# Performance work log

Hardware: AMD Instinct MI355X
Metric: run time of the kernel (lower is better)

The kernel has to match this reference:

```python
import jax, jax.numpy as jnp
import numpy as np

H = 64  # hidden_size
IN = 1  # input_size
OUT = 32  # fc output


def _lstm_layer(x, Wih, Whh, bih, bhh):
    """x: (B,T,D_in). Returns (outputs (B,T,H), final h (B,H)). PyTorch gate order i,f,g,o."""
    B = x.shape[0]
    b = bih + bhh  # (4H,)
    # precompute input contributions for all timesteps: (T,B,4H)
    xW = jnp.einsum('btd,gd->tbg', x, Wih) + b

    def step(carry, xw_t):
        h, c = carry
        gates = xw_t + h @ Whh.T  # (B,4H)
        i, f, g, o = jnp.split(gates, 4, axis=-1)
        i = jax.nn.sigmoid(i)
        f = jax.nn.sigmoid(f)
        g = jnp.tanh(g)
        o = jax.nn.sigmoid(o)
        c = f * c + i * g
        h = o * jnp.tanh(c)
        return (h, c), h

    h0 = jnp.zeros((B, H), dtype=x.dtype)
    c0 = jnp.zeros((B, H), dtype=x.dtype)
    (h_T, _), hs = jax.lax.scan(step, (h0, c0), xW)
    return jnp.swapaxes(hs, 0, 1), h_T


def setup_inputs() -> dict:
    key = jax.random.key(0)
    ks = jax.random.split(key, 11)
    s_ih0 = 1.0 / np.sqrt(H)
    inp = {
        'x': jax.random.normal(ks[0], (2048, 512, IN), dtype=jnp.float32),
        # layer 0: input_size -> H
        'Wih0': jax.random.uniform(ks[1], (4 * H, IN), minval=-s_ih0, maxval=s_ih0),
        'Whh0': jax.random.uniform(ks[2], (4 * H, H), minval=-s_ih0, maxval=s_ih0),
        'bih0': jax.random.uniform(ks[3], (4 * H,), minval=-s_ih0, maxval=s_ih0),
        'bhh0': jax.random.uniform(ks[4], (4 * H,), minval=-s_ih0, maxval=s_ih0),
        # layer 1: H -> H
        'Wih1': jax.random.uniform(ks[5], (4 * H, H), minval=-s_ih0, maxval=s_ih0),
        'Whh1': jax.random.uniform(ks[6], (4 * H, H), minval=-s_ih0, maxval=s_ih0),
        'bih1': jax.random.uniform(ks[7], (4 * H,), minval=-s_ih0, maxval=s_ih0),
        'bhh1': jax.random.uniform(ks[8], (4 * H,), minval=-s_ih0, maxval=s_ih0),
        # fc: H -> 32
        'fcW': jax.random.uniform(ks[9], (OUT, H), minval=-s_ih0, maxval=s_ih0),
        'fcb': jax.random.uniform(ks[10], (OUT,), minval=-s_ih0, maxval=s_ih0),
    }
    return inp


def reference(x, Wih0, Whh0, bih0, bhh0, Wih1, Whh1, bih1, bhh1, fcW, fcb):
    h1_seq, _ = _lstm_layer(x, Wih0, Whh0, bih0, bhh0)
    _, h_last = _lstm_layer(h1_seq, Wih1, Whh1, bih1, bhh1)  # hidden[-1]
    features = jax.nn.relu(h_last @ fcW.T + fcb)  # (B, 32)
    return features
```

## Files before the change

kernel.cpp:

```cpp
#include <hip/hip_runtime.h>
#include <hip/hip_bf16.h>


#define HID 64
#define TSTEPS 512
#define MB 8
#define RS 80

typedef _Float16 f16x8 __attribute__((ext_vector_type(8)));
typedef float f32x4 __attribute__((ext_vector_type(4)));
typedef float f32x2 __attribute__((ext_vector_type(2)));

#define KSIG (-1.44269504089f)
#define KTANH (2.88539008178f)

__global__ __launch_bounds__(512, 2) void lstm_feat_kernel(
    const float* __restrict__ x,
    const float* __restrict__ Wih0, const float* __restrict__ Whh0,
    const float* __restrict__ bih0, const float* __restrict__ bhh0,
    const float* __restrict__ Wih1, const float* __restrict__ Whh1,
    const float* __restrict__ bih1, const float* __restrict__ bhh1,
    const float* __restrict__ fcW, const float* __restrict__ fcb,
    float* __restrict__ out)
{
    __shared__ float x_lds[TSTEPS * MB];
    __shared__ __align__(16) _Float16 h0_lds[2][MB * RS];
    __shared__ __align__(16) _Float16 h1_lds[2][MB * RS];
    __shared__ float h1f32[MB * HID];
    __shared__ float fcw_lds[32 * HID];
    __shared__ float fcb_lds[32];

    const int tid  = threadIdx.x;
    const int wave = tid >> 6;
    const int lane = tid & 63;
    const int nq   = lane & 15;
    const int quad = lane >> 4;
    const bool l0q = quad < 2;
    const bool evn = (nq & 1) == 0;
    const int ucell = wave * 8 + (nq >> 1);
    const int bbase = blockIdx.x * MB;

    for (int i = tid; i < TSTEPS * MB; i += 512) {
        int r = i >> 9, t = i & (TSTEPS - 1);
        x_lds[t * MB + r] = x[(bbase + r) * TSTEPS + t];
    }
    for (int i = tid; i < 32 * HID; i += 512) fcw_lds[i] = fcW[i];
    if (tid < 32) fcb_lds[tid] = fcb[tid];
    for (int i = tid; i < 2 * MB * RS; i += 512) {
        ((_Float16*)h0_lds)[i] = (_Float16)0.f;
        ((_Float16*)h1_lds)[i] = (_Float16)0.f;
    }

    const int nA = (nq & 1) * 64 + ucell;
    const int nB = (2 + (nq & 1)) * 64 + ucell;
    const float kBs = evn ? KTANH : KSIG;
    f16x8 wA0[2], wB0[2], wiA[2], whA[2], wiB[2], whB[2];
    #pragma unroll
    for (int ks = 0; ks < 2; ++ks) {
        const int k0 = quad * 8 + ks * 32;
        f16x8 a, b, c, d, e, f;
        #pragma unroll
        for (int j = 0; j < 8; ++j) {
            a[j] = (_Float16)(KSIG * Whh0[nA * HID + k0 + j]);
            b[j] = (_Float16)(kBs  * Whh0[nB * HID + k0 + j]);
            c[j] = (_Float16)(KSIG * Wih1[nA * HID + k0 + j]);
            d[j] = (_Float16)(KSIG * Whh1[nA * HID + k0 + j]);
            e[j] = (_Float16)(kBs  * Wih1[nB * HID + k0 + j]);
            f[j] = (_Float16)(kBs  * Whh1[nB * HID + k0 + j]);
        }
        wA0[ks] = a; wB0[ks] = b; wiA[ks] = c; whA[ks] = d; wiB[ks] = e; whB[ks] = f;
    }
    const float bA0 = KSIG * (bih0[nA] + bhh0[nA]);
    const float bB0 = kBs  * (bih0[nB] + bhh0[nB]);
    const float bA1 = KSIG * (bih1[nA] + bhh1[nA]);
    const float bB1 = kBs  * (bih1[nB] + bhh1[nB]);
    const float wxA = KSIG * Wih0[nA];
    const float wxB = kBs  * Wih0[nB];

    const float AB = evn ? -2.f : 1.f;
    const float BB = evn ? 1.f : 0.f;

    const f32x4 biasA1 = {bA1, bA1, bA1, bA1};
    const f32x4 biasB1 = {bB1, bB1, bB1, bB1};
    const int arow = (nq & 7) * RS + quad * 8;
    const int xoff = (quad & 1) * 4;

    const int e0 = evn ? 0 : 2;
    const int b0 = (quad * 4 + e0) & 7;
    const int waddr = b0 * RS + ucell;
    _Float16* const hdw[2] = { l0q ? h0_lds[1] : h1_lds[1],
                               l0q ? h0_lds[0] : h1_lds[0] };

    f32x2 cst2 = {0.f, 0.f};
    float hl0 = 0.f, hl1 = 0.f;

    __syncthreads();

    f32x4 cA, cB;
    {
        const float4 xv = *(const float4*)&x_lds[0 * MB + xoff];
        cA[0] = fmaf(xv.x, wxA, bA0); cA[1] = fmaf(xv.y, wxA, bA0);
        cA[2] = fmaf(xv.z, wxA, bA0); cA[3] = fmaf(xv.w, wxA, bA0);
        cB[0] = fmaf(xv.x, wxB, bB0); cB[1] = fmaf(xv.y, wxB, bB0);
        cB[2] = fmaf(xv.z, wxB, bB0); cB[3] = fmaf(xv.w, wxB, bB0);
    }

    auto step = [&](int xk_next, int pp, bool maskK0) {
        const f16x8 a00 = *(const f16x8*)&h0_lds[pp][arow];
        const f16x8 a01 = *(const f16x8*)&h0_lds[pp][arow + 32];
        const f16x8 a10 = *(const f16x8*)&h1_lds[pp][arow];
        const f16x8 a11 = *(const f16x8*)&h1_lds[pp][arow + 32];

        f32x4 tA = __builtin_amdgcn_mfma_f32_16x16x32_f16(a00, wA0[0], cA, 0, 0, 0);
        f32x4 tB = __builtin_amdgcn_mfma_f32_16x16x32_f16(a00, wB0[0], cB, 0, 0, 0);
        f32x4 uA = __builtin_amdgcn_mfma_f32_16x16x32_f16(a00, wiA[0], biasA1, 0, 0, 0);
        f32x4 uB = __builtin_amdgcn_mfma_f32_16x16x32_f16(a00, wiB[0], biasB1, 0, 0, 0);
        tA = __builtin_amdgcn_mfma_f32_16x16x32_f16(a01, wA0[1], tA, 0, 0, 0);
        tB = __builtin_amdgcn_mfma_f32_16x16x32_f16(a01, wB0[1], tB, 0, 0, 0);
        uA = __builtin_amdgcn_mfma_f32_16x16x32_f16(a01, wiA[1], uA, 0, 0, 0);
        uB = __builtin_amdgcn_mfma_f32_16x16x32_f16(a01, wiB[1], uB, 0, 0, 0);
        uA = __builtin_amdgcn_mfma_f32_16x16x32_f16(a10, whA[0], uA, 0, 0, 0);
        uB = __builtin_amdgcn_mfma_f32_16x16x32_f16(a10, whB[0], uB, 0, 0, 0);
        uA = __builtin_amdgcn_mfma_f32_16x16x32_f16(a11, whA[1], uA, 0, 0, 0);
        uB = __builtin_amdgcn_mfma_f32_16x16x32_f16(a11, whB[1], uB, 0, 0, 0);

        {
            const float4 xv = *(const float4*)&x_lds[xk_next * MB + xoff];
            cA[0] = fmaf(xv.x, wxA, bA0); cA[1] = fmaf(xv.y, wxA, bA0);
            cA[2] = fmaf(xv.z, wxA, bA0); cA[3] = fmaf(xv.w, wxA, bA0);
            cB[0] = fmaf(xv.x, wxB, bB0); cB[1] = fmaf(xv.y, wxB, bB0);
            cB[2] = fmaf(xv.z, wxB, bB0); cB[3] = fmaf(xv.w, wxB, bB0);
        }

        const bool docell = maskK0 ? l0q : true;
        if (docell) {
            float sA[4], sB[4];
            #pragma unroll
            for (int r = 0; r < 4; ++r) {
                const float pA = l0q ? tA[r] : uA[r];
                const float pB = l0q ? tB[r] : uB[r];
                sA[r] = __builtin_amdgcn_rcpf(1.f + __builtin_amdgcn_exp2f(pA));
                sB[r] = fmaf(AB, __builtin_amdgcn_rcpf(1.f + __builtin_amdgcn_exp2f(pB)), BB);
            }
            const float rxA0 = __shfl_xor(evn ? sA[2] : sA[0], 1);
            const float rxA1 = __shfl_xor(evn ? sA[3] : sA[1], 1);
            const float rxB0 = __shfl_xor(evn ? sB[2] : sB[0], 1);
            const float rxB1 = __shfl_xor(evn ? sB[3] : sB[1], 1);
            f32x2 iv2, fv2, gv2, ov2;
            iv2.x = evn ? sA[0] : rxA0;  iv2.y = evn ? sA[1] : rxA1;
            fv2.x = evn ? rxA0 : sA[2];  fv2.y = evn ? rxA1 : sA[3];
            gv2.x = evn ? sB[0] : rxB0;  gv2.y = evn ? sB[1] : rxB1;
            ov2.x = evn ? rxB0 : sB[2];  ov2.y = evn ? rxB1 : sB[3];
            cst2 = fv2 * cst2 + iv2 * gv2;
            f32x2 ex, rc;
            ex.x = __builtin_amdgcn_exp2f(KTANH * cst2.x);
            ex.y = __builtin_amdgcn_exp2f(KTANH * cst2.y);
            rc.x = __builtin_amdgcn_rcpf(1.f + ex.x);
            rc.y = __builtin_amdgcn_rcpf(1.f + ex.y);
            const f32x2 th = 1.f - 2.f * rc;
            const f32x2 h2 = ov2 * th;
            hl0 = h2.x; hl1 = h2.y;
            _Float16* hdst = (pp == 0) ? hdw[0] : hdw[1];
            hdst[waddr]      = (_Float16)h2.x;
            hdst[waddr + RS] = (_Float16)h2.y;
        }
        __syncthreads();
    };

    step(1, 0, true);
    for (int k = 1; k < 511; k += 2) {
        step(k + 1, 1, false);
        step(k + 2, 0, false);
    }
    step(511, 1, false);
    step(511, 0, false);

    if (!l0q) {
        h1f32[b0 * HID + ucell]       = hl0;
        h1f32[(b0 + 1) * HID + ucell] = hl1;
    }
    __syncthreads();

    if (tid < MB * 32) {
        const int o  = tid & 31;
        const int rr = tid >> 5;
        float acc = fcb_lds[o];
        #pragma unroll 8
        for (int kk = 0; kk < HID; ++kk)
            acc += h1f32[rr * HID + kk] * fcw_lds[o * HID + kk];
        out[(bbase + rr) * 32 + o] = fmaxf(acc, 0.f);
    }
}

extern "C" void kernel_launch(void* const* d_in, const int* in_sizes, int n_in,
                              void* d_out, int out_size, void* d_ws, size_t ws_size,
                              hipStream_t stream) {
    const float* x    = (const float*)d_in[0];
    const float* Wih0 = (const float*)d_in[1];
    const float* Whh0 = (const float*)d_in[2];
    const float* bih0 = (const float*)d_in[3];
    const float* bhh0 = (const float*)d_in[4];
    const float* Wih1 = (const float*)d_in[5];
    const float* Whh1 = (const float*)d_in[6];
    const float* bih1 = (const float*)d_in[7];
    const float* bhh1 = (const float*)d_in[8];
    const float* fcW  = (const float*)d_in[9];
    const float* fcb  = (const float*)d_in[10];
    float* out = (float*)d_out;

    lstm_feat_kernel<<<2048 / MB, 512, 0, stream>>>(
        x, Wih0, Whh0, bih0, bhh0, Wih1, Whh1, bih1, bhh1, fcW, fcb, out);
}
```

Before: 378.1 us.

## Split gate columns across 16 waves, one gate per lane per MFMA tile

Doubles the block to 1024 threads so each wave handles 4 hidden units with all four gates in one 16-column MFMA tile. Each wave now issues 6 MFMAs per step instead of 12, and each lane updates a single cell state. Gate values are gathered with two xor-shuffle rounds instead of one. The aim is to shorten the per-step serial critical path of the recurrence by spreading work over more waves. The cost is more waves joining each per-step barrier, an extra shuffle round, and lower occupancy per CU.

```diff
diff --git a/kernel.cpp b/kernel.cpp
--- a/kernel.cpp
+++ b/kernel.cpp
@@ -9,12 +9,11 @@
 
 typedef _Float16 f16x8 __attribute__((ext_vector_type(8)));
 typedef float f32x4 __attribute__((ext_vector_type(4)));
-typedef float f32x2 __attribute__((ext_vector_type(2)));
 
 #define KSIG (-1.44269504089f)
 #define KTANH (2.88539008178f)
 
-__global__ __launch_bounds__(512, 2) void lstm_feat_kernel(
+__global__ __launch_bounds__(1024, 4) void lstm_feat_kernel(
     const float* __restrict__ x,
     const float* __restrict__ Wih0, const float* __restrict__ Whh0,
     const float* __restrict__ bih0, const float* __restrict__ bhh0,
@@ -36,73 +35,58 @@
     const int nq   = lane & 15;
     const int quad = lane >> 4;
     const bool l0q = quad < 2;
-    const bool evn = (nq & 1) == 0;
-    const int ucell = wave * 8 + (nq >> 1);
+    const int gate = nq & 3;
+    const int u    = wave * 4 + (nq >> 2);
     const int bbase = blockIdx.x * MB;
 
-    for (int i = tid; i < TSTEPS * MB; i += 512) {
+    for (int i = tid; i < TSTEPS * MB; i += 1024) {
         int r = i >> 9, t = i & (TSTEPS - 1);
         x_lds[t * MB + r] = x[(bbase + r) * TSTEPS + t];
     }
-    for (int i = tid; i < 32 * HID; i += 512) fcw_lds[i] = fcW[i];
+    for (int i = tid; i < 32 * HID; i += 1024) fcw_lds[i] = fcW[i];
     if (tid < 32) fcb_lds[tid] = fcb[tid];
-    for (int i = tid; i < 2 * MB * RS; i += 512) {
+    for (int i = tid; i < 2 * MB * RS; i += 1024) {
         ((_Float16*)h0_lds)[i] = (_Float16)0.f;
         ((_Float16*)h1_lds)[i] = (_Float16)0.f;
     }
 
-    const int nA = (nq & 1) * 64 + ucell;
-    const int nB = (2 + (nq & 1)) * 64 + ucell;
-    const float kBs = evn ? KTANH : KSIG;
-    f16x8 wA0[2], wB0[2], wiA[2], whA[2], wiB[2], whB[2];
+    const int nW = gate * 64 + u;
+    const float kg = (gate == 2) ? KTANH : KSIG;
+    f16x8 wh0[2], wi1[2], wh1[2];
     #pragma unroll
     for (int ks = 0; ks < 2; ++ks) {
         const int k0 = quad * 8 + ks * 32;
-        f16x8 a, b, c, d, e, f;
+        f16x8 a, b, c;
         #pragma unroll
         for (int j = 0; j < 8; ++j) {
-            a[j] = (_Float16)(KSIG * Whh0[nA * HID + k0 + j]);
-            b[j] = (_Float16)(kBs  * Whh0[nB * HID + k0 + j]);
-            c[j] = (_Float16)(KSIG * Wih1[nA * HID + k0 + j]);
-            d[j] = (_Float16)(KSIG * Whh1[nA * HID + k0 + j]);
-            e[j] = (_Float16)(kBs  * Wih1[nB * HID + k0 + j]);
-            f[j] = (_Float16)(kBs  * Whh1[nB * HID + k0 + j]);
+            a[j] = (_Float16)(kg * Whh0[nW * HID + k0 + j]);
+            b[j] = (_Float16)(kg * Wih1[nW * HID + k0 + j]);
+            c[j] = (_Float16)(kg * Whh1[nW * HID + k0 + j]);
         }
-        wA0[ks] = a; wB0[ks] = b; wiA[ks] = c; whA[ks] = d; wiB[ks] = e; whB[ks] = f;
+        wh0[ks] = a; wi1[ks] = b; wh1[ks] = c;
     }
-    const float bA0 = KSIG * (bih0[nA] + bhh0[nA]);
-    const float bB0 = kBs  * (bih0[nB] + bhh0[nB]);
-    const float bA1 = KSIG * (bih1[nA] + bhh1[nA]);
-    const float bB1 = kBs  * (bih1[nB] + bhh1[nB]);
-    const float wxA = KSIG * Wih0[nA];
-    const float wxB = kBs  * Wih0[nB];
+    const float b0c = kg * (bih0[nW] + bhh0[nW]);
+    const float b1c = kg * (bih1[nW] + bhh1[nW]);
+    const float wxc = kg * Wih0[nW];
+    const float Ag = (gate == 2) ? -2.f : 1.f;
+    const float Bg = (gate == 2) ? 1.f : 0.f;
 
-    const float AB = evn ? -2.f : 1.f;
-    const float BB = evn ? 1.f : 0.f;
-
-    const f32x4 biasA1 = {bA1, bA1, bA1, bA1};
-    const f32x4 biasB1 = {bB1, bB1, bB1, bB1};
+    const f32x4 bias1 = {b1c, b1c, b1c, b1c};
     const int arow = (nq & 7) * RS + quad * 8;
     const int xoff = (quad & 1) * 4;
-
-    const int e0 = evn ? 0 : 2;
-    const int b0 = (quad * 4 + e0) & 7;
-    const int waddr = b0 * RS + ucell;
-    _Float16* const hdw[2] = { l0q ? h0_lds[1] : h1_lds[1],
-                               l0q ? h0_lds[0] : h1_lds[0] };
-
-    f32x2 cst2 = {0.f, 0.f};
-    float hl0 = 0.f, hl1 = 0.f;
+    const int bcell = (quad * 4 + gate) & 7;
+    const int waddr = bcell * RS + u;
+    const bool tlo = (gate & 1) != 0;
+    const bool thi = (gate & 2) != 0;
+    float cst = 0.f, hl = 0.f;
 
     __syncthreads();
 
-    f32x4 cA, cB;
+    f32x4 cA;
     {
         const float4 xv = *(const float4*)&x_lds[0 * MB + xoff];
-        cA[0] = fmaf(xv.x, wxA, bA0); cA[1] = fmaf(xv.y, wxA, bA0);
-        cA[2] = fmaf(xv.z, wxA, bA0); cA[3] = fmaf(xv.w, wxA, bA0);
-        cB[0] = fmaf(xv.x, wxB, bB0); cB[1] = fmaf(xv.y, wxB, bB0);
-        cB[2] = fmaf(xv.z, wxB, bB0); cB[3] = fmaf(xv.w, wxB, bB0);
+        cA[0] = fmaf(xv.x, wxc, b0c); cA[1] = fmaf(xv.y, wxc, b0c);
+        cA[2] = fmaf(xv.z, wxc, b0c); cA[3] = fmaf(xv.w, wxc, b0c);
     }
 
     auto step = [&](int xk_next, int pp, bool maskK0) {
@@ -111,58 +95,53 @@
         const f16x8 a10 = *(const f16x8*)&h1_lds[pp][arow];
         const f16x8 a11 = *(const f16x8*)&h1_lds[pp][arow + 32];
 
-        f32x4 tA = __builtin_amdgcn_mfma_f32_16x16x32_f16(a00, wA0[0], cA, 0, 0, 0);
-        f32x4 tB = __builtin_amdgcn_mfma_f32_16x16x32_f16(a00, wB0[0], cB, 0, 0, 0);
-        f32x4 uA = __builtin_amdgcn_mfma_f32_16x16x32_f16(a00, wiA[0], biasA1, 0, 0, 0);
-        f32x4 uB = __builtin_amdgcn_mfma_f32_16x16x32_f16(a00, wiB[0], biasB1, 0, 0, 0);
-        tA = __builtin_amdgcn_mfma_f32_16x16x32_f16(a01, wA0[1], tA, 0, 0, 0);
-        tB = __builtin_amdgcn_mfma_f32_16x16x32_f16(a01, wB0[1], tB, 0, 0, 0);
-        uA = __builtin_amdgcn_mfma_f32_16x16x32_f16(a01, wiA[1], uA, 0, 0, 0);
-        uB = __builtin_amdgcn_mfma_f32_16x16x32_f16(a01, wiB[1], uB, 0, 0, 0);
-        uA = __builtin_amdgcn_mfma_f32_16x16x32_f16(a10, whA[0], uA, 0, 0, 0);
-        uB = __builtin_amdgcn_mfma_f32_16x16x32_f16(a10, whB[0], uB, 0, 0, 0);
-        uA = __builtin_amdgcn_mfma_f32_16x16x32_f16(a11, whA[1], uA, 0, 0, 0);
-        uB = __builtin_amdgcn_mfma_f32_16x16x32_f16(a11, whB[1], uB, 0, 0, 0);
+        f32x4 tA = __builtin_amdgcn_mfma_f32_16x16x32_f16(a00, wh0[0], cA, 0, 0, 0);
+        f32x4 uA = __builtin_amdgcn_mfma_f32_16x16x32_f16(a00, wi1[0], bias1, 0, 0, 0);
+        tA = __builtin_amdgcn_mfma_f32_16x16x32_f16(a01, wh0[1], tA, 0, 0, 0);
+        uA = __builtin_amdgcn_mfma_f32_16x16x32_f16(a01, wi1[1], uA, 0, 0, 0);
+        uA = __builtin_amdgcn_mfma_f32_16x16x32_f16(a10, wh1[0], uA, 0, 0, 0);
+        uA = __builtin_amdgcn_mfma_f32_16x16x32_f16(a11, wh1[1], uA, 0, 0, 0);
 
         {
             const float4 xv = *(const float4*)&x_lds[xk_next * MB + xoff];
-            cA[0] = fmaf(xv.x, wxA, bA0); cA[1] = fmaf(xv.y, wxA, bA0);
-            cA[2] = fmaf(xv.z, wxA, bA0); cA[3] = fmaf(xv.w, wxA, bA0);
-            cB[0] = fmaf(xv.x, wxB, bB0); cB[1] = fmaf(xv.y, wxB, bB0);
-            cB[2] = fmaf(xv.z, wxB, bB0); cB[3] = fmaf(xv.w, wxB, bB0);
+            cA[0] = fmaf(xv.x, wxc, b0c); cA[1] = fmaf(xv.y, wxc, b0c);
+            cA[2] = fmaf(xv.z, wxc, b0c); cA[3] = fmaf(xv.w, wxc, b0c);
         }
 
         const bool docell = maskK0 ? l0q : true;
         if (docell) {
-            float sA[4], sB[4];
-            #pragma unroll
-            for (int r = 0; r < 4; ++r) {
-                const float pA = l0q ? tA[r] : uA[r];
-                const float pB = l0q ? tB[r] : uB[r];
-                sA[r] = __builtin_amdgcn_rcpf(1.f + __builtin_amdgcn_exp2f(pA));
-                sB[r] = fmaf(AB, __builtin_amdgcn_rcpf(1.f + __builtin_amdgcn_exp2f(pB)), BB);
+            float v0, v1, v2, v3;
+            {
+                const float p0 = l0q ? tA[0] : uA[0];
+                const float p1 = l0q ? tA[1] : uA[1];
+                const float p2 = l0q ? tA[2] : uA[2];
+                const float p3 = l0q ? tA[3] : uA[3];
+                v0 = fmaf(Ag, __builtin_amdgcn_rcpf(1.f + __builtin_amdgcn_exp2f(p0)), Bg);
+                v1 = fmaf(Ag, __builtin_amdgcn_rcpf(1.f + __builtin_amdgcn_exp2f(p1)), Bg);
+                v2 = fmaf(Ag, __builtin_amdgcn_rcpf(1.f + __builtin_amdgcn_exp2f(p2)), Bg);
+                v3 = fmaf(Ag, __builtin_amdgcn_rcpf(1.f + __builtin_amdgcn_exp2f(p3)), Bg);
             }
-            const float rxA0 = __shfl_xor(evn ? sA[2] : sA[0], 1);
-            const float rxA1 = __shfl_xor(evn ? sA[3] : sA[1], 1);
-            const float rxB0 = __shfl_xor(evn ? sB[2] : sB[0], 1);
-            const float rxB1 = __shfl_xor(evn ? sB[3] : sB[1], 1);
-            f32x2 iv2, fv2, gv2, ov2;
-            iv2.x = evn ? sA[0] : rxA0;  iv2.y = evn ? sA[1] : rxA1;
-            fv2.x = evn ? rxA0 : sA[2];  fv2.y = evn ? rxA1 : sA[3];
-            gv2.x = evn ? sB[0] : rxB0;  gv2.y = evn ? sB[1] : rxB1;
-            ov2.x = evn ? rxB0 : sB[2];  ov2.y = evn ? rxB1 : sB[3];
-            cst2 = fv2 * cst2 + iv2 * gv2;
-            f32x2 ex, rc;
-            ex.x = __builtin_amdgcn_exp2f(KTANH * cst2.x);
-            ex.y = __builtin_amdgcn_exp2f(KTANH * cst2.y);
-            rc.x = __builtin_amdgcn_rcpf(1.f + ex.x);
-            rc.y = __builtin_amdgcn_rcpf(1.f + ex.y);
-            const f32x2 th = 1.f - 2.f * rc;
-            const f32x2 h2 = ov2 * th;
-            hl0 = h2.x; hl1 = h2.y;
-            _Float16* hdst = (pp == 0) ? hdw[0] : hdw[1];
-            hdst[waddr]      = (_Float16)h2.x;
-            hdst[waddr + RS] = (_Float16)h2.y;
+            {
+                float sa = tlo ? v0 : v1;
+                float sb = tlo ? v2 : v3;
+                const float ra = __shfl_xor(sa, 1);
+                const float rb = __shfl_xor(sb, 1);
+                v0 = tlo ? ra : v0;  v1 = tlo ? v1 : ra;
+                v2 = tlo ? rb : v2;  v3 = tlo ? v3 : rb;
+                sa = thi ? v0 : v2;
+                sb = thi ? v1 : v3;
+                const float rc = __shfl_xor(sa, 2);
+                const float rd = __shfl_xor(sb, 2);
+                v0 = thi ? rc : v0;  v2 = thi ? v2 : rc;
+                v1 = thi ? rd : v1;  v3 = thi ? v3 : rd;
+            }
+            cst = fmaf(v1, cst, v0 * v2);
+            const float th = fmaf(-2.f, __builtin_amdgcn_rcpf(
+                                 1.f + __builtin_amdgcn_exp2f(KTANH * cst)), 1.f);
+            const float h = v3 * th;
+            hl = h;
+            _Float16* hdst = l0q ? h0_lds[pp ^ 1] : h1_lds[pp ^ 1];
+            hdst[waddr] = (_Float16)h;
         }
         __syncthreads();
     };
@@ -175,10 +154,7 @@
     step(511, 1, false);
     step(511, 0, false);
 
-    if (!l0q) {
-        h1f32[b0 * HID + ucell]       = hl0;
-        h1f32[(b0 + 1) * HID + ucell] = hl1;
-    }
+    if (!l0q) h1f32[bcell * HID + u] = hl;
     __syncthreads();
 
     if (tid < MB * 32) {
@@ -208,6 +184,6 @@
     const float* fcb  = (const float*)d_in[10];
     float* out = (float*)d_out;
 
-    lstm_feat_kernel<<<2048 / MB, 512, 0, stream>>>(
+    lstm_feat_kernel<<<2048 / MB, 1024, 0, stream>>>(
         x, Wih0, Whh0, bih0, bhh0, Wih1, Whh1, bih1, bhh1, fcW, fcb, out);
 }
```

Result: slower. 420.3 us (+11.2%).
